# Kernel tuning notes

Hardware: AMD Instinct MI355X
Metric: run time of the kernel (lower is better)

The kernel has to match this reference:

```python
import math
import jax, jax.numpy as jnp
import numpy as np

S = 2048      # seq_length
D = 1024      # embedding_dim
H = 16        # num_qkv_heads
HD = D // H   # head_size = 64
L = 4         # num_hidden_layers
V = 32000     # vocab_size
EPS = 1e-5    # nn.LayerNorm default eps


def setup_inputs() -> dict:
    key = jax.random.key(0)
    ks = jax.random.split(key, 16)
    def n(k, shape, scale=0.02):
        return (jax.random.normal(k, shape, jnp.float32) * scale)
    return {
        "input_ids": jax.random.randint(ks[0], (S,), 0, V),
        "embed":     n(ks[1], (V, D)),
        "pos_enc":   n(ks[2], (S, D)),
        # per-layer stacked params; nn.Linear stores W as [out, in]
        "wq": n(ks[3], (L, D, D)), "bq": jnp.zeros((L, D), jnp.float32),
        "wk": n(ks[4], (L, D, D)), "bk": jnp.zeros((L, D), jnp.float32),
        "wv": n(ks[5], (L, D, D)), "bv": jnp.zeros((L, D), jnp.float32),
        "wo": n(ks[6], (L, D, D)), "bo": jnp.zeros((L, D), jnp.float32),
        "ln1_g": jnp.ones((L, D), jnp.float32), "ln1_b": jnp.zeros((L, D), jnp.float32),
        "w1": n(ks[7], (L, 4 * D, D)), "b1": jnp.zeros((L, 4 * D), jnp.float32),
        "w2": n(ks[8], (L, D, 4 * D)), "b2": jnp.zeros((L, D), jnp.float32),
        "ln2_g": jnp.ones((L, D), jnp.float32), "ln2_b": jnp.zeros((L, D), jnp.float32),
        "lm_head": n(ks[9], (V, D)),
    }


def _layer_norm(x, g, b):
    mu = jnp.mean(x, axis=-1, keepdims=True)
    var = jnp.mean(jnp.square(x - mu), axis=-1, keepdims=True)
    return (x - mu) * jax.lax.rsqrt(var + EPS) * g + b


def _forward(input_ids, embed, pos_enc, wq, bq, wk, bk, wv, bv, wo, bo,
             ln1_g, ln1_b, w1, b1, w2, b2, ln2_g, ln2_b, lm_head):
    s = input_ids.shape[0]
    h = embed[input_ids] + pos_enc[:s]                      # [S, D]
    causal = jnp.tril(jnp.ones((s, s), dtype=bool))         # [S, S]
    inv_sqrt_dk = 1.0 / math.sqrt(HD)

    def layer(h, p):
        (lwq, lbq, lwk, lbk, lwv, lbv, lwo, lbo,
         g1, bn1, lw1, lb1, lw2, lb2, g2, bn2) = p
        q = (h @ lwq.T + lbq).reshape(s, H, HD).transpose(1, 0, 2)  # [H, S, HD]
        k = (h @ lwk.T + lbk).reshape(s, H, HD).transpose(1, 0, 2)
        v = (h @ lwv.T + lbv).reshape(s, H, HD).transpose(1, 0, 2)
        scores = jnp.einsum('hqd,hkd->hqk', q, k) * inv_sqrt_dk     # [H, S, S]
        scores = jnp.where(causal, scores, -jnp.inf)
        attn = jax.nn.softmax(scores, axis=-1)
        o = jnp.einsum('hqk,hkd->hqd', attn, v)                     # [H, S, HD]
        o = o.transpose(1, 0, 2).reshape(s, D) @ lwo.T + lbo        # [S, D]
        h = _layer_norm(h + o, g1, bn1)
        m = jax.nn.relu(h @ lw1.T + lb1) @ lw2.T + lb2              # [S, D]
        h = _layer_norm(h + m, g2, bn2)
        return h, None

    h, _ = jax.lax.scan(layer, h, (wq, bq, wk, bk, wv, bv, wo, bo,
                                   ln1_g, ln1_b, w1, b1, w2, b2, ln2_g, ln2_b))
    return h @ lm_head.T                                    # [S, V] logits


def reference(input_ids, embed, pos_enc, wq, bq, wk, bk, wv, bv, wo, bo,
              ln1_g, ln1_b, w1, b1, w2, b2, ln2_g, ln2_b, lm_head):
    return _forward(input_ids, embed, pos_enc, wq, bq, wk, bk, wv, bv, wo, bo,
                    ln1_g, ln1_b, w1, b1, w2, b2, ln2_g, ln2_b, lm_head)
```

## Files before the change

### kernel.cpp

```cpp
#include <hip/hip_runtime.h>
#include <hip/hip_bf16.h>

#define S 2048
#define D 1024
#define NH 16
#define HD 64
#define NL 4
#define VOCAB 32000
#define DFF 4096
#define EPS_LN 1e-5f

typedef unsigned short ushortT;
typedef __attribute__((ext_vector_type(8))) short short8;
typedef __attribute__((ext_vector_type(4))) unsigned short ushort4v;
typedef __attribute__((ext_vector_type(4))) float f32x4;

__device__ __forceinline__ ushortT f2bf(float f) {
    unsigned u = __float_as_uint(f);
    u += 0x7FFFu + ((u >> 16) & 1u);
    return (ushortT)(u >> 16);
}

__device__ __forceinline__ void gload_lds16(const ushortT* g, ushortT* l) {
    auto gp = (const __attribute__((address_space(1))) unsigned int*)(uintptr_t)g;
    auto lp = (__attribute__((address_space(3))) unsigned int*)(uintptr_t)l;
    __builtin_amdgcn_global_load_lds(gp, lp, 16, 0, 0);
}

__device__ __forceinline__ void cvt8(const float* s, ushortT* d) {
    float4 a = *(const float4*)s;
    float4 b = *(const float4*)(s + 4);
    short8 r;
    r[0] = (short)f2bf(a.x); r[1] = (short)f2bf(a.y);
    r[2] = (short)f2bf(a.z); r[3] = (short)f2bf(a.w);
    r[4] = (short)f2bf(b.x); r[5] = (short)f2bf(b.y);
    r[6] = (short)f2bf(b.z); r[7] = (short)f2bf(b.w);
    *(short8*)d = r;
}

__global__ __launch_bounds__(256) void embed_kernel(
    const int* __restrict__ ids, const float* __restrict__ embed,
    const float* __restrict__ pos, float* __restrict__ hf, ushortT* __restrict__ hb)
{
    int i = blockIdx.x * 256 + threadIdx.x;
    int srow = i >> 10;
    int d = i & (D - 1);
    float v = embed[(size_t)ids[srow] * D + d] + pos[i];
    hf[i] = v;
    hb[i] = f2bf(v);
}

__global__ __launch_bounds__(256) void convert_layer(
    const float* __restrict__ wq, const float* __restrict__ wk, const float* __restrict__ wv,
    const float* __restrict__ wo, const float* __restrict__ w1, const float* __restrict__ w2,
    const float* __restrict__ bq, const float* __restrict__ bk, const float* __restrict__ bv,
    int l, ushortT* __restrict__ wl, float* __restrict__ bqkv)
{
    constexpr int R = (D * D) / 8;
    const int u = blockIdx.x * 256 + threadIdx.x;
    if (u < 12 * R) {
        const float* src;
        if (u < 3 * R) {
            int sub = u >> 17, off = u & (R - 1);
            const float* w = (sub == 0) ? wq : (sub == 1) ? wk : wv;
            src = w + (size_t)l * D * D + (size_t)off * 8;
        } else if (u < 4 * R) {
            src = wo + (size_t)l * D * D + (size_t)(u - 3 * R) * 8;
        } else if (u < 8 * R) {
            src = w1 + (size_t)l * 4 * D * D + (size_t)(u - 4 * R) * 8;
        } else {
            src = w2 + (size_t)l * 4 * D * D + (size_t)(u - 8 * R) * 8;
        }
        cvt8(src, wl + (size_t)u * 8);
    } else if (u < 12 * R + 384) {
        int i = u - 12 * R;
        int sub = i >> 7, off = (i & 127) * 8;
        const float* src = ((sub == 0) ? bq : (sub == 1) ? bk : bv) + (size_t)l * D + off;
        *(float4*)(bqkv + sub * D + off)     = *(const float4*)src;
        *(float4*)(bqkv + sub * D + off + 4) = *(const float4*)(src + 4);
    }
}

__global__ __launch_bounds__(256) void convert_flat(
    const float* __restrict__ src, ushortT* __restrict__ dst)
{
    const size_t u = (size_t)blockIdx.x * 256 + threadIdx.x;
    cvt8(src + u * 8, dst + u * 8);
}

template<int BN, int OUTMODE, int RELU, int HASBIAS>
__global__ __launch_bounds__(256) void gemm_bf(
    const ushortT* __restrict__ A, const ushortT* __restrict__ B,
    const float* __restrict__ bias, void* __restrict__ Cn, void* __restrict__ Ct,
    int N, int K)
{
    constexpr int WN = BN / 2;
    constexpr int NCT = WN / 16;
    __shared__ alignas(16) ushortT As[128 * 32];
    __shared__ alignas(16) ushortT Bs[BN * 32];

    const int tid = threadIdx.x;
    const int id = blockIdx.x;
    const int brow = (id & 15) * 128;
    const int bcol = (id >> 4) * BN;
    const int lane = tid & 63, wid = tid >> 6;
    const int l15 = lane & 15, l4 = lane >> 4;
    const int wr = wid >> 1, wc = wid & 1;
    const int str = tid >> 2;
    const int stc = (tid & 3) * 8;

    f32x4 acc[4][NCT] = {};

    const ushortT* Ab = A + (size_t)(brow + str) * K + stc;
    const ushortT* Bb = B + (size_t)(bcol + str) * K + stc;
    ushortT* AsD = &As[tid * 8];
    ushortT* BsD = &Bs[tid * 8];

    const int nkb = K >> 5;
    for (int kb = 0; kb < nkb; ++kb) {
        const int ko = kb * 32;
        gload_lds16(Ab + ko, AsD);
        gload_lds16(Ab + ko + (size_t)64 * K, AsD + 2048);
        gload_lds16(Bb + ko, BsD);
        if (BN == 128) gload_lds16(Bb + ko + (size_t)64 * K, BsD + 2048);
        __syncthreads();

        short8 af[4], bfr[NCT];
        #pragma unroll
        for (int rt = 0; rt < 4; ++rt)
            af[rt] = *(const short8*)&As[(wr * 64 + rt * 16 + l15) * 32 + l4 * 8];
        #pragma unroll
        for (int ct = 0; ct < NCT; ++ct)
            bfr[ct] = *(const short8*)&Bs[(wc * WN + ct * 16 + l15) * 32 + l4 * 8];
        #pragma unroll
        for (int rt = 0; rt < 4; ++rt)
            #pragma unroll
            for (int ct = 0; ct < NCT; ++ct)
                acc[rt][ct] = __builtin_amdgcn_mfma_f32_16x16x32_bf16(af[rt], bfr[ct], acc[rt][ct], 0, 0, 0);
        __syncthreads();
    }

    #pragma unroll
    for (int rt = 0; rt < 4; ++rt) {
        const int crow0 = brow + wr * 64 + rt * 16 + l4 * 4;
        #pragma unroll
        for (int ct = 0; ct < NCT; ++ct) {
            const int ccol = bcol + wc * WN + ct * 16 + l15;
            const float bv = HASBIAS ? bias[ccol] : 0.0f;
            if (OUTMODE == 0) {
                float* C = (float*)Cn;
                #pragma unroll
                for (int j = 0; j < 4; ++j) {
                    float v = acc[rt][ct][j] + bv;
                    if (RELU) v = fmaxf(v, 0.0f);
                    C[(size_t)(crow0 + j) * N + ccol] = v;
                }
            } else if (OUTMODE == 1) {
                ushortT* C = (ushortT*)Cn;
                #pragma unroll
                for (int j = 0; j < 4; ++j) {
                    float v = acc[rt][ct][j] + bv;
                    if (RELU) v = fmaxf(v, 0.0f);
                    C[(size_t)(crow0 + j) * N + ccol] = f2bf(v);
                }
            }
        }
    }
}

template<int OUTMODE, int RELU, int HASBIAS>
__global__ __launch_bounds__(512) void gemm256v(
    const ushortT* __restrict__ A, const ushortT* __restrict__ B,
    const float* __restrict__ bias, void* __restrict__ Cn, void* __restrict__ Ct,
    int N, int NBn, int Kloop, int stride)
{
    __shared__ alignas(128) ushortT lds[73728];

    const int tid = threadIdx.x;
    const int bid = blockIdx.x;
    const int cpx = gridDim.x >> 3;
    const int wgid = (bid & 7) * cpx + (bid >> 3);
    const int brow = (wgid & 7) << 8;
    const int rest = wgid >> 3;
    const int split = rest / NBn;
    const int bcol = (rest - split * NBn) << 7;
    const int kofs = split * Kloop;

    const int lane = tid & 63, wid = tid >> 6;
    const int l15 = lane & 15, l4 = lane >> 4;
    const int wm = wid >> 1, wn = wid & 1;
    const int NT = Kloop >> 6;

    const int srow = tid >> 3;
    const int scol = ((tid & 7) ^ (srow & 7)) * 8;
    const ushortT* Asrc = A + (size_t)(brow + srow) * stride + kofs + scol;
    const ushortT* Bsrc = B + (size_t)(bcol + srow) * stride + kofs + scol;

    auto stA = [&](int t, int h) {
        if (t < NT) {
            const int sb = t % 3;
            #pragma unroll
            for (int g = 0; g < 2; ++g)
                gload_lds16(Asrc + (size_t)(h * 128 + g * 64) * stride + (size_t)t * 64,
                            &lds[sb * 24576 + h * 8192 + g * 4096 + tid * 8]);
        }
    };
    auto stB = [&](int t) {
        if (t < NT) {
            const int sb = t % 3;
            #pragma unroll
            for (int g = 0; g < 2; ++g)
                gload_lds16(Bsrc + (size_t)(g * 64) * stride + (size_t)t * 64,
                            &lds[sb * 24576 + 16384 + g * 4096 + tid * 8]);
        }
    };

    f32x4 acc[4][4] = {};

    stA(0, 0); stA(0, 1); stB(0);
    stA(1, 0); stA(1, 1); stB(1);
    asm volatile("s_waitcnt vmcnt(6)" ::: "memory");
    __builtin_amdgcn_s_barrier();

    for (int t = 0; t < NT; ++t) {
        const unsigned abase = (unsigned)(t % 3) * 24576;
        short8 af[4][2], bf2[2][2];

        #pragma unroll
        for (int r16 = 0; r16 < 4; ++r16)
            #pragma unroll
            for (int kk = 0; kk < 2; ++kk)
                af[r16][kk] = *(const short8*)&lds[abase +
                    ((wm * 64 + r16 * 16 + l15) << 6) +
                    ((((kk << 2) + l4) ^ (l15 & 7)) << 3)];
        #pragma unroll
        for (int c16 = 0; c16 < 2; ++c16)
            #pragma unroll
            for (int kk = 0; kk < 2; ++kk)
                bf2[c16][kk] = *(const short8*)&lds[abase + 16384 +
                    ((wn * 64 + c16 * 16 + l15) << 6) +
                    ((((kk << 2) + l4) ^ (l15 & 7)) << 3)];
        stA(t + 2, 0); stA(t + 2, 1);
        __builtin_amdgcn_s_barrier();
        asm volatile("s_waitcnt lgkmcnt(0)" ::: "memory");
        __builtin_amdgcn_sched_barrier(0);
        __builtin_amdgcn_s_setprio(1);
        #pragma unroll
        for (int kk = 0; kk < 2; ++kk)
            #pragma unroll
            for (int r16 = 0; r16 < 4; ++r16)
                #pragma unroll
                for (int c16 = 0; c16 < 2; ++c16)
                    acc[r16][c16] = __builtin_amdgcn_mfma_f32_16x16x32_bf16(
                        af[r16][kk], bf2[c16][kk], acc[r16][c16], 0, 0, 0);
        __builtin_amdgcn_s_setprio(0);
        __builtin_amdgcn_s_barrier();

        #pragma unroll
        for (int c16 = 0; c16 < 2; ++c16)
            #pragma unroll
            for (int kk = 0; kk < 2; ++kk)
                bf2[c16][kk] = *(const short8*)&lds[abase + 16384 +
                    ((wn * 64 + (c16 + 2) * 16 + l15) << 6) +
                    ((((kk << 2) + l4) ^ (l15 & 7)) << 3)];
        stB(t + 2);
        __builtin_amdgcn_s_barrier();
        asm volatile("s_waitcnt lgkmcnt(0)" ::: "memory");
        __builtin_amdgcn_sched_barrier(0);
        __builtin_amdgcn_s_setprio(1);
        #pragma unroll
        for (int kk = 0; kk < 2; ++kk)
            #pragma unroll
            for (int r16 = 0; r16 < 4; ++r16)
                #pragma unroll
                for (int c16 = 0; c16 < 2; ++c16)
                    acc[r16][c16 + 2] = __builtin_amdgcn_mfma_f32_16x16x32_bf16(
                        af[r16][kk], bf2[c16][kk], acc[r16][c16 + 2], 0, 0, 0);
        __builtin_amdgcn_s_setprio(0);
        if (t + 2 < NT) { asm volatile("s_waitcnt vmcnt(6)" ::: "memory"); }
        else            { asm volatile("s_waitcnt vmcnt(0)" ::: "memory"); }
        __builtin_amdgcn_s_barrier();
    }

    #pragma unroll
    for (int r16 = 0; r16 < 4; ++r16)
    #pragma unroll
    for (int c16 = 0; c16 < 4; ++c16) {
        const int crow0 = brow + wm * 64 + r16 * 16 + l4 * 4;
        const int ccol  = bcol + wn * 64 + c16 * 16 + l15;
        const float bv = HASBIAS ? bias[ccol] : 0.0f;
        if (OUTMODE == 0) {
            float* C = (float*)Cn;
            #pragma unroll
            for (int j = 0; j < 4; ++j) {
                float v = acc[r16][c16][j] + bv;
                if (RELU) v = fmaxf(v, 0.0f);
                __builtin_nontemporal_store(v, &C[(size_t)(crow0 + j) * N + ccol]);
            }
        } else if (OUTMODE == 1) {
            ushortT* C = (ushortT*)Cn;
            #pragma unroll
            for (int j = 0; j < 4; ++j) {
                float v = acc[r16][c16][j] + bv;
                if (RELU) v = fmaxf(v, 0.0f);
                C[(size_t)(crow0 + j) * N + ccol] = f2bf(v);
            }
        } else if (OUTMODE == 2) {
            if (ccol < 2048) {
                ushortT* C = (ushortT*)Cn;
                #pragma unroll
                for (int j = 0; j < 4; ++j)
                    C[(size_t)(crow0 + j) * 2048 + ccol] = f2bf(acc[r16][c16][j] + bv);
            } else {
                ushortT* C = (ushortT*)Ct;
                ushort4v wv_;
                #pragma unroll
                for (int j = 0; j < 4; ++j) wv_[j] = f2bf(acc[r16][c16][j] + bv);
                *(ushort4v*)&C[(size_t)(ccol - 2048) * S + crow0] = wv_;
            }
        } else {
            float* C = (float*)Cn + (size_t)split * 2048 * N;
            #pragma unroll
            for (int j = 0; j < 4; ++j)
                C[(size_t)(crow0 + j) * N + ccol] = acc[r16][c16][j];
        }
    }
}

__global__ __launch_bounds__(256) void attn_kernel(
    const ushortT* __restrict__ qk, const ushortT* __restrict__ vt,
    ushortT* __restrict__ att)
{
    const int h = blockIdx.y;
    const int q0 = blockIdx.x * 64;
    const int tid = threadIdx.x;
    const int w = tid >> 6, lane = tid & 63;
    const int l15 = lane & 15, l4 = lane >> 4;
    const int qrow0 = q0 + w * 16;

    __shared__ short p_lds[4][16][48];

    short8 aq[2];
    {
        const ushortT* qp = qk + (size_t)(qrow0 + l15) * 2048 + h * HD + l4 * 8;
        aq[0] = *(const short8*)qp;
        aq[1] = *(const short8*)(qp + 32);
    }

    f32x4 o[4] = {};
    float mrow[4], lrow[4];
    #pragma unroll
    for (int j = 0; j < 4; ++j) { mrow[j] = -1e30f; lrow[j] = 0.0f; }

    const int nkb = blockIdx.x * 2 + 2;
    for (int kb32 = 0; kb32 < nkb; ++kb32) {
        const int kb = kb32 * 32;
        f32x4 s[2] = {};
        #pragma unroll
        for (int kh = 0; kh < 2; ++kh) {
            const ushortT* kp = qk + (size_t)(kb + kh * 16 + l15) * 2048 + 1024 + h * HD + l4 * 8;
            short8 b0 = *(const short8*)kp;
            short8 b1 = *(const short8*)(kp + 32);
            s[kh] = __builtin_amdgcn_mfma_f32_16x16x32_bf16(aq[0], b0, s[kh], 0, 0, 0);
            s[kh] = __builtin_amdgcn_mfma_f32_16x16x32_bf16(aq[1], b1, s[kh], 0, 0, 0);
        }
        float fac[4];
        #pragma unroll
        for (int j = 0; j < 4; ++j) {
            const int qg = qrow0 + l4 * 4 + j;
            float v0 = s[0][j] * 0.125f;
            float v1 = s[1][j] * 0.125f;
            if (kb + l15 > qg)      v0 = -1e30f;
            if (kb + 16 + l15 > qg) v1 = -1e30f;
            float bm = fmaxf(v0, v1);
            #pragma unroll
            for (int d_ = 1; d_ < 16; d_ <<= 1) bm = fmaxf(bm, __shfl_xor(bm, d_, 64));
            const float mnew = fmaxf(mrow[j], bm);
            const float f = __expf(mrow[j] - mnew);
            const float p0 = __expf(v0 - mnew);
            const float p1 = __expf(v1 - mnew);
            s[0][j] = p0; s[1][j] = p1;
            float rs = p0 + p1;
            #pragma unroll
            for (int d_ = 1; d_ < 16; d_ <<= 1) rs += __shfl_xor(rs, d_, 64);
            lrow[j] = lrow[j] * f + rs;
            mrow[j] = mnew;
            fac[j] = f;
        }
        #pragma unroll
        for (int c = 0; c < 4; ++c)
            #pragma unroll
            for (int j = 0; j < 4; ++j) o[c][j] *= fac[j];

        #pragma unroll
        for (int kh = 0; kh < 2; ++kh)
            #pragma unroll
            for (int j = 0; j < 4; ++j)
                p_lds[w][l4 * 4 + j][kh * 16 + l15] = (short)f2bf(s[kh][j]);
        short8 pa = *(const short8*)&p_lds[w][l15][l4 * 8];

        #pragma unroll
        for (int c = 0; c < 4; ++c) {
            short8 bv = *(const short8*)(vt + (size_t)(h * HD + c * 16 + l15) * S + kb + l4 * 8);
            o[c] = __builtin_amdgcn_mfma_f32_16x16x32_bf16(pa, bv, o[c], 0, 0, 0);
        }
    }

    #pragma unroll
    for (int c = 0; c < 4; ++c)
        #pragma unroll
        for (int j = 0; j < 4; ++j)
            att[(size_t)(qrow0 + l4 * 4 + j) * D + h * HD + c * 16 + l15] = f2bf(o[c][j] / lrow[j]);
}

template<int NP>
__global__ __launch_bounds__(256) void ln_kernel(
    const float* __restrict__ a,
    const float* __restrict__ p0, const float* __restrict__ p1,
    const float* __restrict__ p2, const float* __restrict__ p3,
    const float* __restrict__ pbias,
    const float* __restrict__ g, const float* __restrict__ bb,
    float* __restrict__ yf, ushortT* __restrict__ yb)
{
    const int row = blockIdx.x;
    const int tid = threadIdx.x;
    const size_t base = (size_t)row * D;
    float x[4]; float s = 0.f, s2 = 0.f;
    #pragma unroll
    for (int i = 0; i < 4; ++i) {
        const int c = tid + i * 256;
        float v = a[base + c] + p0[base + c] + pbias[c];
        if (NP > 1) v += p1[base + c] + p2[base + c] + p3[base + c];
        x[i] = v;
        s += v; s2 += v * v;
    }
    #pragma unroll
    for (int d_ = 1; d_ < 64; d_ <<= 1) {
        s  += __shfl_xor(s,  d_, 64);
        s2 += __shfl_xor(s2, d_, 64);
    }
    __shared__ float rs[4], rs2[4];
    const int wid = tid >> 6, lane = tid & 63;
    if (lane == 0) { rs[wid] = s; rs2[wid] = s2; }
    __syncthreads();
    s = rs[0] + rs[1] + rs[2] + rs[3];
    s2 = rs2[0] + rs2[1] + rs2[2] + rs2[3];
    const float mu = s * (1.0f / D);
    const float var = s2 * (1.0f / D) - mu * mu;
    const float inv = rsqrtf(var + EPS_LN);
    #pragma unroll
    for (int i = 0; i < 4; ++i) {
        const int c = tid + i * 256;
        float v = (x[i] - mu) * inv * g[c] + bb[c];
        yf[base + c] = v;
        yb[base + c] = f2bf(v);
    }
}

extern "C" void kernel_launch(void* const* d_in, const int* in_sizes, int n_in,
                              void* d_out, int out_size, void* d_ws, size_t ws_size,
                              hipStream_t stream) {
    const int*   ids   = (const int*)  d_in[0];
    const float* emb   = (const float*)d_in[1];
    const float* pos   = (const float*)d_in[2];
    const float* wq    = (const float*)d_in[3];
    const float* bq    = (const float*)d_in[4];
    const float* wk    = (const float*)d_in[5];
    const float* bk    = (const float*)d_in[6];
    const float* wv    = (const float*)d_in[7];
    const float* bv    = (const float*)d_in[8];
    const float* wo    = (const float*)d_in[9];
    const float* bo    = (const float*)d_in[10];
    const float* ln1g  = (const float*)d_in[11];
    const float* ln1b  = (const float*)d_in[12];
    const float* w1    = (const float*)d_in[13];
    const float* b1    = (const float*)d_in[14];
    const float* w2    = (const float*)d_in[15];
    const float* b2    = (const float*)d_in[16];
    const float* ln2g  = (const float*)d_in[17];
    const float* ln2b  = (const float*)d_in[18];
    const float* lmh   = (const float*)d_in[19];
    float* out = (float*)d_out;

    const size_t MB = 1024 * 1024;
    char* w = (char*)d_ws;
    float*   h_f32   = (float*)(w);
    float*   h2_f32  = (float*)(w +  8 * MB);
    float*   om2_f32 = (float*)(w + 16 * MB);
    ushortT* h_bf    = (ushortT*)(w + 24 * MB);
    ushortT* h2_bf   = (ushortT*)(w + 28 * MB);
    ushortT* qk_bf   = (ushortT*)(w + 32 * MB);
    ushortT* vt_bf   = (ushortT*)(w + 40 * MB);
    ushortT* att_bf  = (ushortT*)(w + 44 * MB);
    ushortT* m1_bf   = (ushortT*)(w + 48 * MB);
    ushortT* wl      = (ushortT*)(w + 64 * MB);
    float*   bqkv    = (float*)(w + 88 * MB);
    ushortT* lmh_bf  = (ushortT*)(w + 89 * MB);
    float*   parts   = (float*)(w + 155 * MB);

    const bool use_splitk = ws_size >= (size_t)187 * MB;

    ushortT* wqkv_bf = wl;
    ushortT* wo_bf   = wl + (size_t)3 * D * D;
    ushortT* w1_bf   = wl + (size_t)4 * D * D;
    ushortT* w2_bf   = wl + (size_t)8 * D * D;
    const size_t SD = (size_t)S * D;

    embed_kernel<<<(S * D) / 256, 256, 0, stream>>>(ids, emb, pos, h_f32, h_bf);

    for (int l = 0; l < NL; ++l) {
        convert_layer<<<6146, 256, 0, stream>>>(wq, wk, wv, wo, w1, w2, bq, bk, bv, l, wl, bqkv);

        gemm256v<2, 0, 1><<<8 * 24, 512, 0, stream>>>(h_bf, wqkv_bf, bqkv, qk_bf, vt_bf,
                                                      3072, 24, D, D);

        attn_kernel<<<dim3(S / 64, NH), 256, 0, stream>>>(qk_bf, vt_bf, att_bf);

        gemm_bf<64, 0, 0, 0><<<16 * 16, 256, 0, stream>>>(att_bf, wo_bf, nullptr, om2_f32, nullptr, D, D);
        ln_kernel<1><<<S, 256, 0, stream>>>(h_f32, om2_f32, om2_f32, om2_f32, om2_f32,
                                            bo + (size_t)l * D,
                                            ln1g + (size_t)l * D, ln1b + (size_t)l * D, h2_f32, h2_bf);

        gemm256v<1, 1, 1><<<8 * 32, 512, 0, stream>>>(h2_bf, w1_bf, b1 + (size_t)l * DFF, m1_bf, nullptr,
                                                      DFF, 32, D, D);

        if (use_splitk) {
            gemm256v<3, 0, 0><<<8 * 8 * 4, 512, 0, stream>>>(m1_bf, w2_bf, nullptr, parts, nullptr,
                                                             D, 8, D, DFF);
            ln_kernel<4><<<S, 256, 0, stream>>>(h2_f32, parts, parts + SD, parts + 2 * SD, parts + 3 * SD,
                                                b2 + (size_t)l * D,
                                                ln2g + (size_t)l * D, ln2b + (size_t)l * D, h_f32, h_bf);
        } else {
            gemm_bf<64, 0, 0, 0><<<16 * 16, 256, 0, stream>>>(m1_bf, w2_bf, nullptr, om2_f32, nullptr, D, DFF);
            ln_kernel<1><<<S, 256, 0, stream>>>(h2_f32, om2_f32, om2_f32, om2_f32, om2_f32,
                                                b2 + (size_t)l * D,
                                                ln2g + (size_t)l * D, ln2b + (size_t)l * D, h_f32, h_bf);
        }
    }

    convert_flat<<<(VOCAB * D) / (256 * 8), 256, 0, stream>>>(lmh, lmh_bf);
    gemm256v<0, 0, 0><<<8 * 250, 512, 0, stream>>>(h_bf, lmh_bf, nullptr, out, nullptr,
                                                   VOCAB, 250, D, D);
}
```

Before: 1.153 ms.

## Add 256x256-tile LM-head GEMM and swap MFMA operands for vectorized epilogue stores

Adds a dedicated LM-head GEMM kernel that uses 256x256 output tiles with a four-quadrant pipelined schedule, which halves the grid and raises operand reuse per tile for the large vocab projection. It also adds a SWAP template option to the general GEMM that exchanges the MFMA operands, so each lane holds four consecutive output columns. The FFN GEMMs then write with vector stores and load bias as float4. The larger tile raises register pressure, and the new barrier schedule could stall or lower occupancy.

After: 1.142 ms. About the same (-0.9%).

```diff
diff --git a/kernel.cpp b/kernel.cpp
--- a/kernel.cpp
+++ b/kernel.cpp
@@ -168,7 +168,136 @@
     }
 }
 
-template<int OUTMODE, int RELU, int HASBIAS>
+__global__ __launch_bounds__(512) void gemm_lmhead(
+    const ushortT* __restrict__ A, const ushortT* __restrict__ B,
+    float* __restrict__ C, int N)
+{
+    constexpr int K = 1024;
+    constexpr int NT = K >> 6;
+    __shared__ alignas(128) ushortT lds[65536];
+
+    const int tid = threadIdx.x;
+    const int NB = N >> 8;
+    const int bid = blockIdx.x;
+    const int wgid = (bid & 7) * (NB >> 3) * 8 / 8 * 8 + 0;
+    (void)wgid;
+    const int cpx = gridDim.x >> 3;
+    const int wg = (bid & 7) * cpx + (bid >> 3);
+    const int brow = (wg & 7) << 8;
+    const int bcol = (wg >> 3) << 8;
+
+    const int lane = tid & 63;
+    const int wid = tid >> 6;
+    const int l15 = lane & 15, l4 = lane >> 4;
+    const int wm = wid >> 2, wn = wid & 3;
+
+    const int srow = tid >> 3;
+    const int scol = ((tid & 7) ^ (srow & 7)) * 8;
+    const ushortT* Asrc = A + (size_t)(brow + srow) * K + scol;
+    const ushortT* Bsrc = B + (size_t)(bcol + srow) * K + scol;
+
+    auto stA = [&](int t, int h) {
+        if (t < NT) {
+            const int bb = t & 1;
+            #pragma unroll
+            for (int g = 0; g < 2; ++g)
+                gload_lds16(Asrc + (size_t)(h * 128 + g * 64) * K + (size_t)t * 64,
+                            &lds[bb * 32768 + h * 8192 + g * 4096 + tid * 8]);
+        }
+    };
+    auto stB = [&](int t, int h) {
+        if (t < NT) {
+            const int bb = t & 1;
+            #pragma unroll
+            for (int g = 0; g < 2; ++g)
+                gload_lds16(Bsrc + (size_t)(h * 128 + g * 64) * K + (size_t)t * 64,
+                            &lds[bb * 32768 + 16384 + h * 8192 + g * 4096 + tid * 8]);
+        }
+    };
+
+    f32x4 acc[2][2][4][2] = {};
+
+    stA(0, 0); stB(0, 0); stA(0, 1); stB(0, 1); stB(1, 0); stA(1, 0);
+    asm volatile("s_waitcnt vmcnt(4)" ::: "memory");
+    __builtin_amdgcn_s_barrier();
+
+#define RD_A(DST, RC)                                                          \
+    _Pragma("unroll") for (int r16 = 0; r16 < 4; ++r16)                        \
+    _Pragma("unroll") for (int kk = 0; kk < 2; ++kk)                           \
+        DST[r16][kk] = *(const short8*)&lds[b * 32768 +                        \
+            (((RC) * 128 + wm * 64 + r16 * 16 + l15) << 6) +                   \
+            ((((kk << 2) + l4) ^ (l15 & 7)) << 3)];
+#define RD_B(DST, CC)                                                          \
+    _Pragma("unroll") for (int c16 = 0; c16 < 2; ++c16)                        \
+    _Pragma("unroll") for (int kk = 0; kk < 2; ++kk)                           \
+        DST[c16][kk] = *(const short8*)&lds[b * 32768 + 16384 +                \
+            (((CC) * 128 + wn * 32 + c16 * 16 + l15) << 6) +                   \
+            ((((kk << 2) + l4) ^ (l15 & 7)) << 3)];
+#define MFMA_Q(AF, BF, RC, CC)                                                 \
+    __builtin_amdgcn_s_setprio(1);                                             \
+    _Pragma("unroll") for (int kk = 0; kk < 2; ++kk)                           \
+    _Pragma("unroll") for (int r16 = 0; r16 < 4; ++r16)                        \
+    _Pragma("unroll") for (int c16 = 0; c16 < 2; ++c16)                        \
+        acc[RC][CC][r16][c16] = __builtin_amdgcn_mfma_f32_16x16x32_bf16(       \
+            BF[c16][kk], AF[r16][kk], acc[RC][CC][r16][c16], 0, 0, 0);         \
+    __builtin_amdgcn_s_setprio(0);
+#define WAIT_LGKM                                                              \
+    asm volatile("s_waitcnt lgkmcnt(0)" ::: "memory");                         \
+    __builtin_amdgcn_sched_barrier(0);
+
+    for (int t = 0; t < NT; ++t) {
+        const int b = t & 1;
+        short8 a_[4][2], b0[2][2], b1[2][2];
+
+        RD_A(a_, 0); RD_B(b0, 0);
+        stA(t + 1, 1);
+        __builtin_amdgcn_s_barrier();
+        WAIT_LGKM;
+        MFMA_Q(a_, b0, 0, 0);
+        __builtin_amdgcn_s_barrier();
+
+        RD_B(b1, 1);
+        stB(t + 1, 1);
+        __builtin_amdgcn_s_barrier();
+        WAIT_LGKM;
+        MFMA_Q(a_, b1, 0, 1);
+        __builtin_amdgcn_s_barrier();
+
+        RD_A(a_, 1);
+        stB(t + 2, 0);
+        __builtin_amdgcn_s_barrier();
+        WAIT_LGKM;
+        MFMA_Q(a_, b1, 1, 1);
+        __builtin_amdgcn_s_barrier();
+
+        stA(t + 2, 0);
+        __builtin_amdgcn_s_barrier();
+        MFMA_Q(a_, b0, 1, 0);
+        if (t < NT - 2) { asm volatile("s_waitcnt vmcnt(4)" ::: "memory"); }
+        else            { asm volatile("s_waitcnt vmcnt(0)" ::: "memory"); }
+        __builtin_amdgcn_s_barrier();
+    }
+#undef RD_A
+#undef RD_B
+#undef MFMA_Q
+#undef WAIT_LGKM
+
+    #pragma unroll
+    for (int rc = 0; rc < 2; ++rc)
+    #pragma unroll
+    for (int cc = 0; cc < 2; ++cc)
+    #pragma unroll
+    for (int r16 = 0; r16 < 4; ++r16)
+    #pragma unroll
+    for (int c16 = 0; c16 < 2; ++c16) {
+        const int row = brow + rc * 128 + wm * 64 + r16 * 16 + l15;
+        const int col = bcol + cc * 128 + wn * 32 + c16 * 16 + l4 * 4;
+        __builtin_nontemporal_store(acc[rc][cc][r16][c16],
+                                    (f32x4*)&C[(size_t)row * N + col]);
+    }
+}
+
+template<int OUTMODE, int RELU, int HASBIAS, int SWAP>
 __global__ __launch_bounds__(512) void gemm256v(
     const ushortT* __restrict__ A, const ushortT* __restrict__ B,
     const float* __restrict__ bias, void* __restrict__ Cn, void* __restrict__ Ct,
@@ -251,8 +380,9 @@
             for (int r16 = 0; r16 < 4; ++r16)
                 #pragma unroll
                 for (int c16 = 0; c16 < 2; ++c16)
-                    acc[r16][c16] = __builtin_amdgcn_mfma_f32_16x16x32_bf16(
-                        af[r16][kk], bf2[c16][kk], acc[r16][c16], 0, 0, 0);
+                    acc[r16][c16] = SWAP
+                        ? __builtin_amdgcn_mfma_f32_16x16x32_bf16(bf2[c16][kk], af[r16][kk], acc[r16][c16], 0, 0, 0)
+                        : __builtin_amdgcn_mfma_f32_16x16x32_bf16(af[r16][kk], bf2[c16][kk], acc[r16][c16], 0, 0, 0);
         __builtin_amdgcn_s_setprio(0);
         __builtin_amdgcn_s_barrier();
 
@@ -274,8 +404,9 @@
             for (int r16 = 0; r16 < 4; ++r16)
                 #pragma unroll
                 for (int c16 = 0; c16 < 2; ++c16)
-                    acc[r16][c16 + 2] = __builtin_amdgcn_mfma_f32_16x16x32_bf16(
-                        af[r16][kk], bf2[c16][kk], acc[r16][c16 + 2], 0, 0, 0);
+                    acc[r16][c16 + 2] = SWAP
+                        ? __builtin_amdgcn_mfma_f32_16x16x32_bf16(bf2[c16][kk], af[r16][kk], acc[r16][c16 + 2], 0, 0, 0)
+                        : __builtin_amdgcn_mfma_f32_16x16x32_bf16(af[r16][kk], bf2[c16][kk], acc[r16][c16 + 2], 0, 0, 0);
         __builtin_amdgcn_s_setprio(0);
         if (t + 2 < NT) { asm volatile("s_waitcnt vmcnt(6)" ::: "memory"); }
         else            { asm volatile("s_waitcnt vmcnt(0)" ::: "memory"); }
@@ -286,43 +417,63 @@
     for (int r16 = 0; r16 < 4; ++r16)
     #pragma unroll
     for (int c16 = 0; c16 < 4; ++c16) {
-        const int crow0 = brow + wm * 64 + r16 * 16 + l4 * 4;
-        const int ccol  = bcol + wn * 64 + c16 * 16 + l15;
-        const float bv = HASBIAS ? bias[ccol] : 0.0f;
-        if (OUTMODE == 0) {
-            float* C = (float*)Cn;
-            #pragma unroll
-            for (int j = 0; j < 4; ++j) {
-                float v = acc[r16][c16][j] + bv;
-                if (RELU) v = fmaxf(v, 0.0f);
-                __builtin_nontemporal_store(v, &C[(size_t)(crow0 + j) * N + ccol]);
+        if (SWAP) {
+            const int row = brow + wm * 64 + r16 * 16 + l15;
+            const int col = bcol + wn * 64 + c16 * 16 + l4 * 4;
+            f32x4 v = acc[r16][c16];
+            if (HASBIAS) {
+                float4 b4 = *(const float4*)&bias[col];
+                v[0] += b4.x; v[1] += b4.y; v[2] += b4.z; v[3] += b4.w;
             }
-        } else if (OUTMODE == 1) {
-            ushortT* C = (ushortT*)Cn;
-            #pragma unroll
-            for (int j = 0; j < 4; ++j) {
-                float v = acc[r16][c16][j] + bv;
-                if (RELU) v = fmaxf(v, 0.0f);
-                C[(size_t)(crow0 + j) * N + ccol] = f2bf(v);
+            if (RELU) {
+                #pragma unroll
+                for (int j = 0; j < 4; ++j) v[j] = fmaxf(v[j], 0.0f);
             }
-        } else if (OUTMODE == 2) {
-            if (ccol < 2048) {
-                ushortT* C = (ushortT*)Cn;
-                #pragma unroll
-                for (int j = 0; j < 4; ++j)
-                    C[(size_t)(crow0 + j) * 2048 + ccol] = f2bf(acc[r16][c16][j] + bv);
+            if (OUTMODE == 1) {
+                ushort4v o;
+                #pragma unroll
+                for (int j = 0; j < 4; ++j) o[j] = f2bf(v[j]);
+                *(ushort4v*)&((ushortT*)Cn)[(size_t)row * N + col] = o;
+            } else if (OUTMODE == 3) {
+                float* C = (float*)Cn + (size_t)split * 2048 * N;
+                *(f32x4*)&C[(size_t)row * N + col] = v;
             } else {
-                ushortT* C = (ushortT*)Ct;
-                ushort4v wv_;
-                #pragma unroll
-                for (int j = 0; j < 4; ++j) wv_[j] = f2bf(acc[r16][c16][j] + bv);
-                *(ushort4v*)&C[(size_t)(ccol - 2048) * S + crow0] = wv_;
+                __builtin_nontemporal_store(v, (f32x4*)&((float*)Cn)[(size_t)row * N + col]);
             }
         } else {
-            float* C = (float*)Cn + (size_t)split * 2048 * N;
-            #pragma unroll
-            for (int j = 0; j < 4; ++j)
-                C[(size_t)(crow0 + j) * N + ccol] = acc[r16][c16][j];
+            const int crow0 = brow + wm * 64 + r16 * 16 + l4 * 4;
+            const int ccol  = bcol + wn * 64 + c16 * 16 + l15;
+            const float bv = HASBIAS ? bias[ccol] : 0.0f;
+            if (OUTMODE == 2) {
+                if (ccol < 2048) {
+                    ushortT* C = (ushortT*)Cn;
+                    #pragma unroll
+                    for (int j = 0; j < 4; ++j)
+                        C[(size_t)(crow0 + j) * 2048 + ccol] = f2bf(acc[r16][c16][j] + bv);
+                } else {
+                    ushortT* C = (ushortT*)Ct;
+                    ushort4v wv_;
+                    #pragma unroll
+                    for (int j = 0; j < 4; ++j) wv_[j] = f2bf(acc[r16][c16][j] + bv);
+                    *(ushort4v*)&C[(size_t)(ccol - 2048) * S + crow0] = wv_;
+                }
+            } else if (OUTMODE == 1) {
+                ushortT* C = (ushortT*)Cn;
+                #pragma unroll
+                for (int j = 0; j < 4; ++j) {
+                    float v = acc[r16][c16][j] + bv;
+                    if (RELU) v = fmaxf(v, 0.0f);
+                    C[(size_t)(crow0 + j) * N + ccol] = f2bf(v);
+                }
+            } else {
+                float* C = (float*)Cn;
+                #pragma unroll
+                for (int j = 0; j < 4; ++j) {
+                    float v = acc[r16][c16][j] + bv;
+                    if (RELU) v = fmaxf(v, 0.0f);
+                    C[(size_t)(crow0 + j) * N + ccol] = v;
+                }
+            }
         }
     }
 }
@@ -511,8 +662,8 @@
     for (int l = 0; l < NL; ++l) {
         convert_layer<<<6146, 256, 0, stream>>>(wq, wk, wv, wo, w1, w2, bq, bk, bv, l, wl, bqkv);
 
-        gemm256v<2, 0, 1><<<8 * 24, 512, 0, stream>>>(h_bf, wqkv_bf, bqkv, qk_bf, vt_bf,
-                                                      3072, 24, D, D);
+        gemm256v<2, 0, 1, 0><<<8 * 24, 512, 0, stream>>>(h_bf, wqkv_bf, bqkv, qk_bf, vt_bf,
+                                                         3072, 24, D, D);
 
         attn_kernel<<<dim3(S / 64, NH), 256, 0, stream>>>(qk_bf, vt_bf, att_bf);
 
@@ -521,12 +672,12 @@
                                             bo + (size_t)l * D,
                                             ln1g + (size_t)l * D, ln1b + (size_t)l * D, h2_f32, h2_bf);
 
-        gemm256v<1, 1, 1><<<8 * 32, 512, 0, stream>>>(h2_bf, w1_bf, b1 + (size_t)l * DFF, m1_bf, nullptr,
-                                                      DFF, 32, D, D);
+        gemm256v<1, 1, 1, 1><<<8 * 32, 512, 0, stream>>>(h2_bf, w1_bf, b1 + (size_t)l * DFF, m1_bf, nullptr,
+                                                         DFF, 32, D, D);
 
         if (use_splitk) {
-            gemm256v<3, 0, 0><<<8 * 8 * 4, 512, 0, stream>>>(m1_bf, w2_bf, nullptr, parts, nullptr,
-                                                             D, 8, D, DFF);
+            gemm256v<3, 0, 0, 1><<<8 * 8 * 4, 512, 0, stream>>>(m1_bf, w2_bf, nullptr, parts, nullptr,
+                                                                D, 8, D, DFF);
             ln_kernel<4><<<S, 256, 0, stream>>>(h2_f32, parts, parts + SD, parts + 2 * SD, parts + 3 * SD,
                                                 b2 + (size_t)l * D,
                                                 ln2g + (size_t)l * D, ln2b + (size_t)l * D, h_f32, h_bf);
@@ -539,6 +690,5 @@
     }
 
     convert_flat<<<(VOCAB * D) / (256 * 8), 256, 0, stream>>>(lmh, lmh_bf);
-    gemm256v<0, 0, 0><<<8 * 250, 512, 0, stream>>>(h_bf, lmh_bf, nullptr, out, nullptr,
-                                                   VOCAB, 250, D, D);
-}
+    gemm_lmhead<<<8 * 125, 512, 0, stream>>>(h_bf, lmh_bf, out, VOCAB);
+}
```
